# Performance work log

Measured on AMD Instinct MI355X. Metric: run time of the kernel, lower is better.

The kernel has to match this reference:

```python
import jax, jax.numpy as jnp
import numpy as np

VOC_SHAPE = (100, 100, 100)   # m_k factors of voc_size = 1_000_000
EMB_SHAPE = (4, 4, 8)         # n_k factors of emb_size = 128
RANK = 16
PAD_IDX = 0
VOC = int(np.prod(VOC_SHAPE))
EMB = int(np.prod(EMB_SHAPE))


def setup_inputs() -> dict:
    key = jax.random.key(0)
    k0, k1, k2, kx = jax.random.split(key, 4)
    # TT-matrix cores [r_k, m_k, n_k, r_{k+1}], boundary ranks = 1.
    # Per-core std chosen so the reconstructed table has stddev near
    # target_stddev = sqrt(2/voc_size) (the 'nn' init intent); exact init
    # distribution is irrelevant to the math being tested.
    d = 3
    target_std = np.sqrt(2.0 / VOC)
    core_std = float((target_std / RANK ** ((d - 1) / 2.0)) ** (1.0 / d))
    core0 = jax.random.normal(k0, (1, VOC_SHAPE[0], EMB_SHAPE[0], RANK), jnp.float32) * core_std
    core1 = jax.random.normal(k1, (RANK, VOC_SHAPE[1], EMB_SHAPE[1], RANK), jnp.float32) * core_std
    core2 = jax.random.normal(k2, (RANK, VOC_SHAPE[2], EMB_SHAPE[2], 1), jnp.float32) * core_std
    x = jax.random.randint(kx, (64, 512), 0, VOC, dtype=jnp.int64)
    return {"x": x, "core0": core0, "core1": core1, "core2": core2}


def _tt_full(core0, core1, core2):
    # Sequential TT-matrix contraction, as in sample_full():
    # res accumulates shape (m1*n1*...*mk*nk, r_{k+1})
    res = core0.reshape(-1, core0.shape[-1])                      # (m1*n1, r1)
    res = res @ core1.reshape(core1.shape[0], -1)                 # (m1*n1, m2*n2*r2)
    res = res.reshape(-1, core2.shape[0]) @ core2.reshape(core2.shape[0], -1)
    # (m1, n1, m2, n2, m3, n3) -> (m1, m2, m3, n1, n2, n3) -> (VOC, EMB)
    m1, m2, m3 = VOC_SHAPE
    n1, n2, n3 = EMB_SHAPE
    full = res.reshape(m1, n1, m2, n2, m3, n3)
    full = full.transpose(0, 2, 4, 1, 3, 5).reshape(VOC, EMB)
    return full


def reference(x, core0, core1, core2):
    xshape = x.shape
    x_flat = x.reshape(-1)
    full = _tt_full(core0, core1, core2)          # [VOC, EMB] materialized table
    rows = full[x_flat]                           # gather [B*S, EMB]
    rows = jnp.where(x_flat[:, None] != PAD_IDX, rows, jnp.zeros_like(rows))
    return rows.reshape(*xshape, EMB)
```

## Files before the change

### kernel.cpp

```cpp
#include <hip/hip_runtime.h>
#include <hip/hip_bf16.h>


#define LDS_PER_WAVE 704

__global__ __launch_bounds__(256) void tt_embed_kernel(
    const int* __restrict__ x,
    const float* __restrict__ c0,
    const float* __restrict__ c1,
    const float* __restrict__ c2,
    float* __restrict__ out,
    int nTok)
{
    __shared__ float lds[4 * LDS_PER_WAVE];
    const int wave = threadIdx.x >> 6;
    const int lane = threadIdx.x & 63;
    const int t = blockIdx.x * 4 + wave;
    const bool active = (t < nTok);

    float* As = lds + wave * LDS_PER_WAVE;
    float* Cs = As + 64;
    float* Ms = Cs + 128;

    int idx = 0;
    if (active) idx = x[t];
    const int i1 = idx / 10000;
    const int rem = idx - i1 * 10000;
    const int i2 = rem / 100;
    const int i3 = rem - i2 * 100;

    if (active) {
        if (lane < 16) {
            ((float4*)As)[lane] = *(const float4*)(c0 + i1 * 64 + lane * 4);
        } else if (lane < 48) {
            const int l = lane - 16;
            const int r2 = l >> 1;
            const int half = l & 1;
            ((float4*)Cs)[l] = *(const float4*)(c2 + (r2 * 100 + i3) * 8 + half * 4);
        }
    }

    const int r1 = lane >> 2;
    const int j2 = lane & 3;
    float bb[16];
    if (active) {
        const float4* bp = (const float4*)(c1 + ((r1 * 100 + i2) * 4 + j2) * 16);
        float4 b0 = bp[0], b1 = bp[1], b2 = bp[2], b3 = bp[3];
        bb[0]=b0.x; bb[1]=b0.y; bb[2]=b0.z; bb[3]=b0.w;
        bb[4]=b1.x; bb[5]=b1.y; bb[6]=b1.z; bb[7]=b1.w;
        bb[8]=b2.x; bb[9]=b2.y; bb[10]=b2.z; bb[11]=b2.w;
        bb[12]=b3.x; bb[13]=b3.y; bb[14]=b3.z; bb[15]=b3.w;
    } else {
        #pragma unroll
        for (int j = 0; j < 16; ++j) bb[j] = 0.0f;
    }

    __syncthreads();

    float mv[8];
    #pragma unroll
    for (int j = 0; j < 8; ++j) mv[j] = 0.0f;
    #pragma unroll
    for (int r2 = 0; r2 < 16; ++r2) {
        const float4* cp = (const float4*)(Cs + r2 * 8);
        float4 ca = cp[0];
        float4 cb = cp[1];
        const float b = bb[r2];
        mv[0] += b * ca.x; mv[1] += b * ca.y; mv[2] += b * ca.z; mv[3] += b * ca.w;
        mv[4] += b * cb.x; mv[5] += b * cb.y; mv[6] += b * cb.z; mv[7] += b * cb.w;
    }
    {
        float4* mp = (float4*)(Ms + lane * 8);
        mp[0] = make_float4(mv[0], mv[1], mv[2], mv[3]);
        mp[1] = make_float4(mv[4], mv[5], mv[6], mv[7]);
    }

    __syncthreads();

    const int e0 = lane * 2;
    const int j1 = e0 >> 5;
    const int mcol = e0 & 31;

    const float4* ap = (const float4*)(As + j1 * 16);
    float4 a0 = ap[0], a1 = ap[1], a2 = ap[2], a3 = ap[3];
    float av[16] = { a0.x, a0.y, a0.z, a0.w, a1.x, a1.y, a1.z, a1.w,
                     a2.x, a2.y, a2.z, a2.w, a3.x, a3.y, a3.z, a3.w };

    float o0 = 0.0f, o1 = 0.0f;
    #pragma unroll
    for (int r = 0; r < 16; ++r) {
        const float2 m = *(const float2*)(Ms + r * 32 + mcol);
        o0 += av[r] * m.x;
        o1 += av[r] * m.y;
    }

    if (idx == 0) { o0 = 0.0f; o1 = 0.0f; }

    if (active) {
        *(float2*)(out + (long)t * 128 + e0) = make_float2(o0, o1);
    }
}

extern "C" void kernel_launch(void* const* d_in, const int* in_sizes, int n_in,
                              void* d_out, int out_size, void* d_ws, size_t ws_size,
                              hipStream_t stream) {
    const int*   x  = (const int*)d_in[0];
    const float* c0 = (const float*)d_in[1];
    const float* c1 = (const float*)d_in[2];
    const float* c2 = (const float*)d_in[3];
    float* out = (float*)d_out;

    const int nTok = out_size / 128;
    const int blocks = (nTok + 3) / 4;
    tt_embed_kernel<<<dim3(blocks), dim3(256), 0, stream>>>(x, c0, c1, c2, out, nTok);
}
```

Before: 80.31 us.

## Load TT cores directly from global, drop block barriers, pad LDS stride

Each wave now loads core0 and core2 slices straight from global memory (core2 via wave-uniform scalar addressing after readfirstlane) instead of staging them in LDS. The two __syncthreads barriers are replaced by a per-wave lgkmcnt wait, since each wave only exchanges data through its own LDS region. The intermediate matrix gets a padded stride of 12 to cut LDS bank conflicts. The risk is that relying on lgkmcnt alone without a wave barrier may not be a sufficient ordering guarantee. Inactive-token guards on the loads are also removed, so out-of-range waves load using index 0.

```diff
diff --git a/kernel.cpp b/kernel.cpp
--- a/kernel.cpp
+++ b/kernel.cpp
@@ -1,8 +1,8 @@
 #include <hip/hip_runtime.h>
-#include <hip/hip_bf16.h>
 
 
-#define LDS_PER_WAVE 704
+#define MS_STRIDE 12
+#define LDS_PER_WAVE (64 * MS_STRIDE)
 
 __global__ __launch_bounds__(256) void tt_embed_kernel(
     const int* __restrict__ x,
@@ -12,84 +12,64 @@
     float* __restrict__ out,
     int nTok)
 {
-    __shared__ float lds[4 * LDS_PER_WAVE];
+    __shared__ __align__(16) float lds[4 * LDS_PER_WAVE];
     const int wave = threadIdx.x >> 6;
     const int lane = threadIdx.x & 63;
     const int t = blockIdx.x * 4 + wave;
     const bool active = (t < nTok);
 
-    float* As = lds + wave * LDS_PER_WAVE;
-    float* Cs = As + 64;
-    float* Ms = Cs + 128;
+    float* Ms = lds + wave * LDS_PER_WAVE;
 
     int idx = 0;
     if (active) idx = x[t];
+    idx = __builtin_amdgcn_readfirstlane(idx);
     const int i1 = idx / 10000;
     const int rem = idx - i1 * 10000;
     const int i2 = rem / 100;
     const int i3 = rem - i2 * 100;
 
-    if (active) {
-        if (lane < 16) {
-            ((float4*)As)[lane] = *(const float4*)(c0 + i1 * 64 + lane * 4);
-        } else if (lane < 48) {
-            const int l = lane - 16;
-            const int r2 = l >> 1;
-            const int half = l & 1;
-            ((float4*)Cs)[l] = *(const float4*)(c2 + (r2 * 100 + i3) * 8 + half * 4);
-        }
-    }
-
     const int r1 = lane >> 2;
     const int j2 = lane & 3;
-    float bb[16];
-    if (active) {
-        const float4* bp = (const float4*)(c1 + ((r1 * 100 + i2) * 4 + j2) * 16);
-        float4 b0 = bp[0], b1 = bp[1], b2 = bp[2], b3 = bp[3];
-        bb[0]=b0.x; bb[1]=b0.y; bb[2]=b0.z; bb[3]=b0.w;
-        bb[4]=b1.x; bb[5]=b1.y; bb[6]=b1.z; bb[7]=b1.w;
-        bb[8]=b2.x; bb[9]=b2.y; bb[10]=b2.z; bb[11]=b2.w;
-        bb[12]=b3.x; bb[13]=b3.y; bb[14]=b3.z; bb[15]=b3.w;
-    } else {
-        #pragma unroll
-        for (int j = 0; j < 16; ++j) bb[j] = 0.0f;
-    }
+    const float4* bp = (const float4*)(c1 + ((r1 * 100 + i2) * 4 + j2) * 16);
+    float4 b0 = bp[0], b1 = bp[1], b2 = bp[2], b3 = bp[3];
 
-    __syncthreads();
+    const int e0 = lane * 2;
+    const int j1 = e0 >> 5;
+    const int mcol = e0 & 31;
+    const float4* ap = (const float4*)(c0 + i1 * 64 + j1 * 16);
+    float4 a0 = ap[0], a1 = ap[1], a2 = ap[2], a3 = ap[3];
+
+    float bb[16] = { b0.x,b0.y,b0.z,b0.w, b1.x,b1.y,b1.z,b1.w,
+                     b2.x,b2.y,b2.z,b2.w, b3.x,b3.y,b3.z,b3.w };
 
     float mv[8];
     #pragma unroll
     for (int j = 0; j < 8; ++j) mv[j] = 0.0f;
+    const float* Cb = c2 + i3 * 8;
     #pragma unroll
     for (int r2 = 0; r2 < 16; ++r2) {
-        const float4* cp = (const float4*)(Cs + r2 * 8);
-        float4 ca = cp[0];
-        float4 cb = cp[1];
+        const float* cp = Cb + r2 * 800;
         const float b = bb[r2];
-        mv[0] += b * ca.x; mv[1] += b * ca.y; mv[2] += b * ca.z; mv[3] += b * ca.w;
-        mv[4] += b * cb.x; mv[5] += b * cb.y; mv[6] += b * cb.z; mv[7] += b * cb.w;
+        mv[0] += b * cp[0]; mv[1] += b * cp[1]; mv[2] += b * cp[2]; mv[3] += b * cp[3];
+        mv[4] += b * cp[4]; mv[5] += b * cp[5]; mv[6] += b * cp[6]; mv[7] += b * cp[7];
     }
+
     {
-        float4* mp = (float4*)(Ms + lane * 8);
+        float4* mp = (float4*)(Ms + lane * MS_STRIDE);
         mp[0] = make_float4(mv[0], mv[1], mv[2], mv[3]);
         mp[1] = make_float4(mv[4], mv[5], mv[6], mv[7]);
     }
 
-    __syncthreads();
+    asm volatile("s_waitcnt lgkmcnt(0)" ::: "memory");
 
-    const int e0 = lane * 2;
-    const int j1 = e0 >> 5;
-    const int mcol = e0 & 31;
+    float av[16] = { a0.x,a0.y,a0.z,a0.w, a1.x,a1.y,a1.z,a1.w,
+                     a2.x,a2.y,a2.z,a2.w, a3.x,a3.y,a3.z,a3.w };
 
-    const float4* ap = (const float4*)(As + j1 * 16);
-    float4 a0 = ap[0], a1 = ap[1], a2 = ap[2], a3 = ap[3];
-    float av[16] = { a0.x, a0.y, a0.z, a0.w, a1.x, a1.y, a1.z, a1.w,
-                     a2.x, a2.y, a2.z, a2.w, a3.x, a3.y, a3.z, a3.w };
-
+    const int rbase = (mcol >> 3) * MS_STRIDE + (mcol & 7);
     float o0 = 0.0f, o1 = 0.0f;
     #pragma unroll
     for (int r = 0; r < 16; ++r) {
-        const float2 m = *(const float2*)(Ms + r * 32 + mcol);
+        const float2 m = *(const float2*)(Ms + r * (4 * MS_STRIDE) + rbase);
         o0 += av[r] * m.x;
         o1 += av[r] * m.y;
     }
```

After: 77.56 us. -3.4%, faster.
